# Optimization experiments

Hardware: AMD Instinct MI355X
Metric: run time of the kernel (lower is better)

Reference implementation:

```python
import jax, jax.numpy as jnp
import numpy as np

N_NODES = 50000


def _relgraphconv(x, W, Wloop, b, src, dst, etypes, n_nodes):
    # DGL RelGraphConv (regularizer=None, self_loop=True, norm=None):
    # out[i] = sum over incoming edges (j->i, rel r) of W_r @ x[j]  +  W_loop @ x[i]  +  b
    # low-mem form: transform all nodes per relation, then gather per edge.
    h_rel = jnp.einsum('ni,rio->rno', x, W)          # [R, N, out]
    msg = h_rel[etypes, src]                          # [E, out]
    agg = jax.ops.segment_sum(msg, dst, num_segments=n_nodes)  # [N, out]
    return agg + x @ Wloop + b


def setup_inputs() -> dict:
    key = jax.random.key(0)
    ks = jax.random.split(key, 12)
    N, E, n_state = N_NODES, 800000, 128
    inp = {
        'x': jax.random.normal(ks[0], (N, n_state), dtype=jnp.float32),
        'src': jax.random.randint(ks[1], (E,), 0, N, dtype=jnp.int32),
        'dst': jax.random.randint(ks[2], (E,), 0, N, dtype=jnp.int32),
        'etypes': jax.random.randint(ks[3], (E,), 0, 2, dtype=jnp.int32),
        'cell_size': jax.random.randint(ks[4], (N,), 0, 8, dtype=jnp.int32),
        'max_size': jax.random.randint(ks[5], (N,), 0, 8, dtype=jnp.int32),
        'W1': jax.random.normal(ks[6], (2, n_state, 64), dtype=jnp.float32) * 0.05,
        'loop1': jax.random.normal(ks[7], (n_state, 64), dtype=jnp.float32) * 0.05,
        'b1': jnp.zeros((64,), dtype=jnp.float32),
        'W2': jax.random.normal(ks[8], (2, 64, 64), dtype=jnp.float32) * 0.05,
        'loop2': jax.random.normal(ks[9], (64, 64), dtype=jnp.float32) * 0.05,
        'b2': jnp.zeros((64,), dtype=jnp.float32),
        'W3': jax.random.normal(ks[10], (2, 64, 2), dtype=jnp.float32) * 0.05,
        'loop3': jax.random.normal(ks[11], (64, 2), dtype=jnp.float32) * 0.05,
        'b3': jnp.zeros((2,), dtype=jnp.float32),
    }
    return inp


def reference(x, src, dst, etypes, cell_size, max_size,
              W1, loop1, b1, W2, loop2, b2, W3, loop3, b3):
    N = x.shape[0]
    h = jax.nn.relu(_relgraphconv(x, W1, loop1, b1, src, dst, etypes, N))
    h = jax.nn.relu(_relgraphconv(h, W2, loop2, b2, src, dst, etypes, N))
    h = _relgraphconv(h, W3, loop3, b3, src, dst, etypes, N)   # [N, 2]
    # action mask: col 0 = cannot upsize, col 1 = cannot downsize
    upper = cell_size >= (max_size - 1)
    lower = cell_size == 0
    mask = jnp.stack([upper, lower], axis=1)                   # [N, 2] bool
    return jnp.where(mask, h.min() - 1.0, h)
```

## Files before the change

kernel.cpp:

```cpp
#include <hip/hip_runtime.h>


#define STRIDE 64
#define BINCAP 2560

typedef unsigned short ushortT;
typedef __attribute__((ext_vector_type(8))) short short8;
typedef __attribute__((ext_vector_type(4))) float f32x4;

__device__ inline ushortT f2bf(float f) {
    union { float f; unsigned u; } v; v.f = f;
    unsigned r = v.u + 0x7FFFu + ((v.u >> 16) & 1u);
    return (ushortT)(r >> 16);
}
__device__ inline float bf2f(ushortT h) {
    union { unsigned u; float f; } v; v.u = ((unsigned)h) << 16;
    return v.f;
}

__device__ inline void atomicMinF(float* addr, float v) {
    if (v >= 0.f) atomicMin((int*)addr, __float_as_int(v));
    else          atomicMax((unsigned int*)addr, __float_as_uint(v));
}

__global__ __launch_bounds__(256) void pack_init_kernel(
    const float* __restrict__ W1, const float* __restrict__ loop1,
    const float* __restrict__ W2, const float* __restrict__ loop2,
    ushortT* __restrict__ BP1, ushortT* __restrict__ BP2,
    int* __restrict__ bincnt, float* __restrict__ minval, int NBINS) {
    int g = (int)blockIdx.x * 256 + (int)threadIdx.x;
    if (g < NBINS) bincnt[g] = 0;
    if (g == 0) *(int*)minval = 0x7f7f7f7f;
    if (g < 3072) {
        int l = g & 63, ks = (g >> 6) & 3, ct = g >> 8;
        int c = ct * 16 + (l & 15);
        int mat = c >> 6, cc = c & 63;
        int kbase = ks * 32 + (l >> 4) * 8;
        ushortT* dstp = BP1 + (size_t)g * 8;
#pragma unroll
        for (int j = 0; j < 8; ++j) {
            int k = kbase + j;
            float v = (mat < 2) ? W1[((size_t)mat * 128 + k) * 64 + cc]
                                : loop1[(size_t)k * 64 + cc];
            dstp[j] = f2bf(v);
        }
    } else {
        int s = g - 3072;
        int l = s & 63, ks = (s >> 6) & 1, ct = s >> 7;
        int c = ct * 16 + (l & 15);
        int mat = c >> 6, cc = c & 63;
        int kbase = ks * 32 + (l >> 4) * 8;
        ushortT* dstp = BP2 + (size_t)s * 8;
#pragma unroll
        for (int j = 0; j < 8; ++j) {
            int k = kbase + j;
            float v = (mat < 2) ? W2[((size_t)mat * 64 + k) * 64 + cc]
                                : loop2[(size_t)k * 64 + cc];
            dstp[j] = f2bf(v);
        }
    }
}

__global__ __launch_bounds__(256) void k1_kernel(
    const float* __restrict__ x, const ushortT* __restrict__ BP1,
    const float* __restrict__ b1,
    ushortT* __restrict__ hrelb, ushortT* __restrict__ H1b,
    const int* __restrict__ src, const int* __restrict__ dst,
    const int* __restrict__ et, int* __restrict__ bincnt, int2* __restrict__ binbuf,
    int N, int E, int NBINS, int NBA) {
    __shared__ int hist[512];
    __shared__ int gbase[512];
    __shared__ ushortT rnk[4096];

    const int t = (int)threadIdx.x;

    if ((int)blockIdx.x < NBA) {
        for (int i = t; i < NBINS; i += 256) hist[i] = 0;
        __syncthreads();
        const int base = (int)blockIdx.x * 4096;
#pragma unroll
        for (int i = 0; i < 16; ++i) {
            int e = base + t + i * 256;
            if (e < E) {
                int bb = dst[e] >> 7;
                rnk[t + i * 256] = (ushortT)atomicAdd(&hist[bb], 1);
            }
        }
        __syncthreads();
        for (int i = t; i < NBINS; i += 256) {
            int h = hist[i];
            gbase[i] = h ? atomicAdd(&bincnt[i], h) : 0;
        }
        __syncthreads();
#pragma unroll
        for (int i = 0; i < 16; ++i) {
            int e = base + t + i * 256;
            if (e < E) {
                int dd = dst[e];
                int bb = dd >> 7;
                int v = et[e] * N + src[e];
                int pos = gbase[bb] + (int)rnk[t + i * 256];
                if (pos < BINCAP)
                    binbuf[(size_t)bb * BINCAP + pos] = make_int2(dd, v);
            }
        }
        return;
    }
    const int w = t >> 6, lane = t & 63;
    const int rowbase = (((int)blockIdx.x - NBA) * 4 + w) * 16;
    const int m = lane & 15, quad = lane >> 4;
    const int nclamp = min(rowbase + m, N - 1);

    short8 a[4];
    const float* xp = x + (size_t)nclamp * 128 + quad * 8;
#pragma unroll
    for (int ks = 0; ks < 4; ++ks) {
        float4 g0 = *(const float4*)(xp + ks * 32);
        float4 g1 = *(const float4*)(xp + ks * 32 + 4);
        a[ks][0] = (short)f2bf(g0.x); a[ks][1] = (short)f2bf(g0.y);
        a[ks][2] = (short)f2bf(g0.z); a[ks][3] = (short)f2bf(g0.w);
        a[ks][4] = (short)f2bf(g1.x); a[ks][5] = (short)f2bf(g1.y);
        a[ks][6] = (short)f2bf(g1.z); a[ks][7] = (short)f2bf(g1.w);
    }

    f32x4 acc[12];
#pragma unroll
    for (int ct = 0; ct < 12; ++ct) acc[ct] = (f32x4){0.f, 0.f, 0.f, 0.f};

#pragma unroll
    for (int ks = 0; ks < 4; ++ks) {
#pragma unroll
        for (int ct = 0; ct < 12; ++ct) {
            short8 b = *(const short8*)&BP1[((size_t)(ct * 4 + ks) * 64 + lane) * 8];
            acc[ct] = __builtin_amdgcn_mfma_f32_16x16x32_bf16(a[ks], b, acc[ct], 0, 0, 0);
        }
    }

    const int node0 = rowbase + quad * 4;
#pragma unroll
    for (int ct = 0; ct < 12; ++ct) {
        int c = ct * 16 + m;
        int mat = c >> 6, cc = c & 63;
        float bias = (mat == 2) ? b1[cc] : 0.f;
#pragma unroll
        for (int j = 0; j < 4; ++j) {
            int n = node0 + j;
            if (n < N) {
                float v = acc[ct][j] + bias;
                if (mat < 2) hrelb[((size_t)mat * N + n) * 64 + cc] = f2bf(v);
                else         H1b[(size_t)n * 64 + cc] = f2bf(v);
            }
        }
    }
}

__global__ __launch_bounds__(256) void phaseB_kernel(
    const int* __restrict__ bincnt, const int2* __restrict__ binbuf,
    int* __restrict__ cnt, int* __restrict__ eidx, int N) {
    __shared__ int lcnt[128];
    const int b = (int)blockIdx.x;
    const int t = (int)threadIdx.x;
    if (t < 128) lcnt[t] = 0;
    __syncthreads();
    const int cb = min(bincnt[b], BINCAP);
    const int2* buf = binbuf + (size_t)b * BINCAP;
    for (int i = t; i < cb; i += 256) {
        int2 rec = buf[i];
        int r = atomicAdd(&lcnt[rec.x & 127], 1);
        if (r < STRIDE) eidx[(size_t)rec.x * STRIDE + r] = rec.y;
    }
    __syncthreads();
    int node = b * 128 + t;
    if (t < 128 && node < N) cnt[node] = min(lcnt[t], STRIDE);
}

__global__ void agg1_kernel(const ushortT* __restrict__ hrelb, const int* __restrict__ eidx,
                            const int* __restrict__ cnt, ushortT* __restrict__ H1b, int N) {
    int node = (int)blockIdx.x * 4 + ((int)threadIdx.x >> 6);
    if (node >= N) return;
    int lane = (int)threadIdx.x & 63;
    int deg = cnt[node];
    int my = (lane < deg) ? eidx[(size_t)node * STRIDE + lane] : 0;
    float acc = bf2f(H1b[(size_t)node * 64 + lane]);
    int j = 0;
    for (; j + 7 < deg; j += 8) {
        int id[8];
        float v[8];
#pragma unroll
        for (int q = 0; q < 8; ++q) id[q] = __shfl(my, j + q, 64);
#pragma unroll
        for (int q = 0; q < 8; ++q) v[q] = bf2f(hrelb[(size_t)id[q] * 64 + lane]);
        acc += ((v[0] + v[1]) + (v[2] + v[3])) + ((v[4] + v[5]) + (v[6] + v[7]));
    }
    for (; j < deg; ++j)
        acc += bf2f(hrelb[(size_t)__shfl(my, j, 64) * 64 + lane]);
    H1b[(size_t)node * 64 + lane] = f2bf(fmaxf(acc, 0.f));
}

__global__ __launch_bounds__(256) void gemm2_mfma(
    const ushortT* __restrict__ H1b, const ushortT* __restrict__ BP2,
    const float* __restrict__ b2,
    ushortT* __restrict__ hrel2b, ushortT* __restrict__ H2b, int N) {
    const int w = (int)threadIdx.x >> 6, lane = (int)threadIdx.x & 63;
    const int rowbase = ((int)blockIdx.x * 4 + w) * 16;
    const int m = lane & 15, quad = lane >> 4;
    const int nclamp = min(rowbase + m, N - 1);

    short8 a[2];
    const ushortT* hp = H1b + (size_t)nclamp * 64 + quad * 8;
    a[0] = *(const short8*)(hp);
    a[1] = *(const short8*)(hp + 32);

    f32x4 acc[12];
#pragma unroll
    for (int ct = 0; ct < 12; ++ct) acc[ct] = (f32x4){0.f, 0.f, 0.f, 0.f};

#pragma unroll
    for (int ks = 0; ks < 2; ++ks) {
#pragma unroll
        for (int ct = 0; ct < 12; ++ct) {
            short8 b = *(const short8*)&BP2[((size_t)(ct * 2 + ks) * 64 + lane) * 8];
            acc[ct] = __builtin_amdgcn_mfma_f32_16x16x32_bf16(a[ks], b, acc[ct], 0, 0, 0);
        }
    }

    const int node0 = rowbase + quad * 4;
#pragma unroll
    for (int ct = 0; ct < 12; ++ct) {
        int c = ct * 16 + m;
        int mat = c >> 6, cc = c & 63;
        float bias = (mat == 2) ? b2[cc] : 0.f;
#pragma unroll
        for (int j = 0; j < 4; ++j) {
            int n = node0 + j;
            if (n < N) {
                float v = acc[ct][j] + bias;
                if (mat < 2) hrel2b[((size_t)mat * N + n) * 64 + cc] = f2bf(v);
                else         H2b[(size_t)n * 64 + cc] = f2bf(v);
            }
        }
    }
}

__global__ void k3_kernel(const ushortT* __restrict__ hrel2b, const ushortT* __restrict__ H2b,
                          const int* __restrict__ eidx, const int* __restrict__ cnt,
                          const float* __restrict__ W3, const float* __restrict__ loop3,
                          const float* __restrict__ b3,
                          float* __restrict__ hrel3, float* __restrict__ H3, int N) {
    int node = (int)blockIdx.x * 4 + ((int)threadIdx.x >> 6);
    if (node >= N) return;
    int lane = (int)threadIdx.x & 63;
    int deg = cnt[node];
    int my = (lane < deg) ? eidx[(size_t)node * STRIDE + lane] : 0;
    float acc = bf2f(H2b[(size_t)node * 64 + lane]);
    int j = 0;
    for (; j + 7 < deg; j += 8) {
        int id[8];
        float v[8];
#pragma unroll
        for (int q = 0; q < 8; ++q) id[q] = __shfl(my, j + q, 64);
#pragma unroll
        for (int q = 0; q < 8; ++q) v[q] = bf2f(hrel2b[(size_t)id[q] * 64 + lane]);
        acc += ((v[0] + v[1]) + (v[2] + v[3])) + ((v[4] + v[5]) + (v[6] + v[7]));
    }
    for (; j < deg; ++j)
        acc += bf2f(hrel2b[(size_t)__shfl(my, j, 64) * 64 + lane]);
    float xk = fmaxf(acc, 0.f);
    float p[6];
    p[0] = xk * W3[lane * 2 + 0];
    p[1] = xk * W3[lane * 2 + 1];
    p[2] = xk * W3[(64 + lane) * 2 + 0];
    p[3] = xk * W3[(64 + lane) * 2 + 1];
    p[4] = xk * loop3[lane * 2 + 0];
    p[5] = xk * loop3[lane * 2 + 1];
#pragma unroll
    for (int mm = 32; mm >= 1; mm >>= 1) {
#pragma unroll
        for (int q = 0; q < 6; ++q) p[q] += __shfl_xor(p[q], mm, 64);
    }
    if (lane == 0) {
        hrel3[(size_t)node * 2 + 0] = p[0];
        hrel3[(size_t)node * 2 + 1] = p[1];
        hrel3[((size_t)N + node) * 2 + 0] = p[2];
        hrel3[((size_t)N + node) * 2 + 1] = p[3];
        H3[(size_t)node * 2 + 0] = p[4] + b3[0];
        H3[(size_t)node * 2 + 1] = p[5] + b3[1];
    }
}

__global__ void agg3min_kernel(const float* __restrict__ hrel3, const int* __restrict__ eidx,
                               const int* __restrict__ cnt, float* __restrict__ H3,
                               float* __restrict__ minval, int N) {
    int n = (int)blockIdx.x * 256 + (int)threadIdx.x;
    float v = 3.4e38f;
    if (n < N) {
        float a0 = H3[n * 2 + 0], a1 = H3[n * 2 + 1];
        int deg = cnt[n];
        const int* row = &eidx[(size_t)n * STRIDE];
        int j = 0;
        for (; j + 3 < deg; j += 4) {
            int i0 = row[j], i1 = row[j + 1], i2 = row[j + 2], i3 = row[j + 3];
            float2 q0 = *(const float2*)&hrel3[(size_t)i0 * 2];
            float2 q1 = *(const float2*)&hrel3[(size_t)i1 * 2];
            float2 q2 = *(const float2*)&hrel3[(size_t)i2 * 2];
            float2 q3 = *(const float2*)&hrel3[(size_t)i3 * 2];
            a0 += (q0.x + q1.x) + (q2.x + q3.x);
            a1 += (q0.y + q1.y) + (q2.y + q3.y);
        }
        for (; j < deg; ++j) {
            float2 q = *(const float2*)&hrel3[(size_t)row[j] * 2];
            a0 += q.x; a1 += q.y;
        }
        H3[n * 2 + 0] = a0;
        H3[n * 2 + 1] = a1;
        v = fminf(a0, a1);
    }
#pragma unroll
    for (int mm = 32; mm >= 1; mm >>= 1) v = fminf(v, __shfl_xor(v, mm, 64));
    __shared__ float s[4];
    if ((threadIdx.x & 63) == 0) s[threadIdx.x >> 6] = v;
    __syncthreads();
    if (threadIdx.x == 0)
        atomicMinF(minval, fminf(fminf(s[0], s[1]), fminf(s[2], s[3])));
}

__global__ void mask_kernel(const float* __restrict__ H3, const float* __restrict__ minval,
                            const int* __restrict__ cs, const int* __restrict__ ms,
                            float* __restrict__ out, int N) {
    int n = (int)blockIdx.x * 256 + (int)threadIdx.x;
    if (n >= N) return;
    float m = minval[0] - 1.0f;
    bool up = cs[n] >= ms[n] - 1;
    bool lo = cs[n] == 0;
    out[n * 2 + 0] = up ? m : H3[n * 2 + 0];
    out[n * 2 + 1] = lo ? m : H3[n * 2 + 1];
}

extern "C" void kernel_launch(void* const* d_in, const int* in_sizes, int n_in,
                              void* d_out, int out_size, void* d_ws, size_t ws_size,
                              hipStream_t stream) {
    const float* x     = (const float*)d_in[0];
    const int* src     = (const int*)d_in[1];
    const int* dst     = (const int*)d_in[2];
    const int* etypes  = (const int*)d_in[3];
    const int* cellsz  = (const int*)d_in[4];
    const int* maxsz   = (const int*)d_in[5];
    const float* W1    = (const float*)d_in[6];
    const float* loop1 = (const float*)d_in[7];
    const float* b1    = (const float*)d_in[8];
    const float* W2    = (const float*)d_in[9];
    const float* loop2 = (const float*)d_in[10];
    const float* b2    = (const float*)d_in[11];
    const float* W3    = (const float*)d_in[12];
    const float* loop3 = (const float*)d_in[13];
    const float* b3    = (const float*)d_in[14];
    float* out = (float*)d_out;

    const int N = in_sizes[0] / 128;
    const int E = in_sizes[1];

    char* p = (char*)d_ws;
    auto alloc = [&](size_t bytes) -> void* {
        void* r = (void*)p;
        p += ((bytes + 255) / 256) * 256;
        return r;
    };
    ushortT* hrelb  = (ushortT*)alloc((size_t)2 * N * 64 * 2);
    ushortT* H1b    = (ushortT*)alloc((size_t)N * 64 * 2);
    ushortT* hrel2b = (ushortT*)alloc((size_t)2 * N * 64 * 2);
    ushortT* H2b    = (ushortT*)alloc((size_t)N * 64 * 2);
    float* hrel3    = (float*)alloc((size_t)2 * N * 2 * 4);
    float* H3       = (float*)alloc((size_t)N * 2 * 4);
    int* cnt        = (int*)alloc((size_t)N * 4);
    int* eidx       = (int*)alloc((size_t)N * STRIDE * 4);
    ushortT* BP1    = (ushortT*)alloc((size_t)3072 * 8 * 2);
    ushortT* BP2    = (ushortT*)alloc((size_t)1536 * 8 * 2);
    float* minval   = (float*)alloc(4);

    const int NBINS = (N + 127) >> 7;
    int* bincnt     = (int*)alloc((size_t)NBINS * 4);
    int2* binbuf    = (int2*)alloc((size_t)NBINS * BINCAP * 8);
    (void)ws_size; (void)n_in; (void)out_size;

    const int NB_N   = (N + 255) / 256;
    const int NTILES = (N + 63) / 64;
    const int NB_W   = (N + 3) / 4;
    const int NBA    = (E + 4095) / 4096;

    pack_init_kernel<<<18, 256, 0, stream>>>(
        W1, loop1, W2, loop2, BP1, BP2, bincnt, minval, NBINS);

    k1_kernel<<<NBA + NTILES, 256, 0, stream>>>(
        x, BP1, b1, hrelb, H1b,
        src, dst, etypes, bincnt, binbuf, N, E, NBINS, NBA);

    phaseB_kernel<<<NBINS, 256, 0, stream>>>(bincnt, binbuf, cnt, eidx, N);

    agg1_kernel<<<NB_W, 256, 0, stream>>>(hrelb, eidx, cnt, H1b, N);

    gemm2_mfma<<<NTILES, 256, 0, stream>>>(H1b, BP2, b2, hrel2b, H2b, N);

    k3_kernel<<<NB_W, 256, 0, stream>>>(hrel2b, H2b, eidx, cnt, W3, loop3, b3,
                                        hrel3, H3, N);

    agg3min_kernel<<<NB_N, 256, 0, stream>>>(hrel3, eidx, cnt, H3, minval, N);
    mask_kernel<<<NB_N, 256, 0, stream>>>(H3, minval, cellsz, maxsz, out, N);
}
```

Baseline: 220.4 us.

## Fuse edge binning, layer-1 aggregation and layer-2 GEMM; fuse final min with mask

```diff
diff --git a/kernel.cpp b/kernel.cpp
--- a/kernel.cpp
+++ b/kernel.cpp
@@ -27,10 +27,11 @@
     const float* __restrict__ W1, const float* __restrict__ loop1,
     const float* __restrict__ W2, const float* __restrict__ loop2,
     ushortT* __restrict__ BP1, ushortT* __restrict__ BP2,
-    int* __restrict__ bincnt, float* __restrict__ minval, int NBINS) {
+    int* __restrict__ bincnt, float* __restrict__ minval,
+    int* __restrict__ done, int NBINS) {
     int g = (int)blockIdx.x * 256 + (int)threadIdx.x;
     if (g < NBINS) bincnt[g] = 0;
-    if (g == 0) *(int*)minval = 0x7f7f7f7f;
+    if (g == 0) { *(int*)minval = 0x7f7f7f7f; *done = 0; }
     if (g < 3072) {
         int l = g & 63, ks = (g >> 6) & 3, ct = g >> 8;
         int c = ct * 16 + (l & 15);
@@ -154,79 +155,95 @@
     }
 }
 
-__global__ __launch_bounds__(256) void phaseB_kernel(
+__global__ __launch_bounds__(512, 4) void ag2_kernel(
+    const ushortT* __restrict__ hrelb, const ushortT* __restrict__ H1b,
+    const ushortT* __restrict__ BP2, const float* __restrict__ b2,
     const int* __restrict__ bincnt, const int2* __restrict__ binbuf,
-    int* __restrict__ cnt, int* __restrict__ eidx, int N) {
-    __shared__ int lcnt[128];
-    const int b = (int)blockIdx.x;
+    int* __restrict__ eidx, int* __restrict__ cnt,
+    ushortT* __restrict__ hrel2b, ushortT* __restrict__ H2b, int N) {
+    __shared__ int lcnt[64];
+    __shared__ int lidx[64][STRIDE];
+    __shared__ __align__(16) ushortT Hs[64][72];
+
     const int t = (int)threadIdx.x;
-    if (t < 128) lcnt[t] = 0;
-    __syncthreads();
-    const int cb = min(bincnt[b], BINCAP);
-    const int2* buf = binbuf + (size_t)b * BINCAP;
-    for (int i = t; i < cb; i += 256) {
+    const int B = (int)blockIdx.x;
+    const int nodeBase = B * 64;
+    const int bin = B >> 1;
+
+    if (t < 64) lcnt[t] = 0;
+    __syncthreads();
+
+    const int cb = min(bincnt[bin], BINCAP);
+    const int2* buf = binbuf + (size_t)bin * BINCAP;
+    for (int i = t; i < cb; i += 512) {
         int2 rec = buf[i];
-        int r = atomicAdd(&lcnt[rec.x & 127], 1);
-        if (r < STRIDE) eidx[(size_t)rec.x * STRIDE + r] = rec.y;
-    }
-    __syncthreads();
-    int node = b * 128 + t;
-    if (t < 128 && node < N) cnt[node] = min(lcnt[t], STRIDE);
-}
-
-__global__ void agg1_kernel(const ushortT* __restrict__ hrelb, const int* __restrict__ eidx,
-                            const int* __restrict__ cnt, ushortT* __restrict__ H1b, int N) {
-    int node = (int)blockIdx.x * 4 + ((int)threadIdx.x >> 6);
-    if (node >= N) return;
-    int lane = (int)threadIdx.x & 63;
-    int deg = cnt[node];
-    int my = (lane < deg) ? eidx[(size_t)node * STRIDE + lane] : 0;
-    float acc = bf2f(H1b[(size_t)node * 64 + lane]);
-    int j = 0;
-    for (; j + 7 < deg; j += 8) {
-        int id[8];
-        float v[8];
-#pragma unroll
-        for (int q = 0; q < 8; ++q) id[q] = __shfl(my, j + q, 64);
-#pragma unroll
-        for (int q = 0; q < 8; ++q) v[q] = bf2f(hrelb[(size_t)id[q] * 64 + lane]);
-        acc += ((v[0] + v[1]) + (v[2] + v[3])) + ((v[4] + v[5]) + (v[6] + v[7]));
-    }
-    for (; j < deg; ++j)
-        acc += bf2f(hrelb[(size_t)__shfl(my, j, 64) * 64 + lane]);
-    H1b[(size_t)node * 64 + lane] = f2bf(fmaxf(acc, 0.f));
-}
-
-__global__ __launch_bounds__(256) void gemm2_mfma(
-    const ushortT* __restrict__ H1b, const ushortT* __restrict__ BP2,
-    const float* __restrict__ b2,
-    ushortT* __restrict__ hrel2b, ushortT* __restrict__ H2b, int N) {
-    const int w = (int)threadIdx.x >> 6, lane = (int)threadIdx.x & 63;
-    const int rowbase = ((int)blockIdx.x * 4 + w) * 16;
+        int local = rec.x - nodeBase;
+        if ((unsigned)local < 64u) {
+            int r = atomicAdd(&lcnt[local], 1);
+            if (r < STRIDE) {
+                lidx[local][r] = rec.y;
+                eidx[(size_t)rec.x * STRIDE + r] = rec.y;
+            }
+        }
+    }
+    __syncthreads();
+    if (t < 64) {
+        int c = min(lcnt[t], STRIDE);
+        lcnt[t] = c;
+        int node = nodeBase + t;
+        if (node < N) cnt[node] = c;
+    }
+    __syncthreads();
+
+    const int w = t >> 6, lane = t & 63;
+
+    for (int i = 0; i < 8; ++i) {
+        int local = w * 8 + i;
+        int node = nodeBase + local;
+        if (node >= N) { Hs[local][lane] = 0; continue; }
+        int deg = lcnt[local];
+        float acc = bf2f(H1b[(size_t)node * 64 + lane]);
+        int j = 0;
+        for (; j + 7 < deg; j += 8) {
+            float v[8];
+#pragma unroll
+            for (int q = 0; q < 8; ++q) {
+                int id = lidx[local][j + q];
+                v[q] = bf2f(hrelb[(size_t)id * 64 + lane]);
+            }
+            acc += ((v[0] + v[1]) + (v[2] + v[3])) + ((v[4] + v[5]) + (v[6] + v[7]));
+        }
+        for (; j < deg; ++j)
+            acc += bf2f(hrelb[(size_t)lidx[local][j] * 64 + lane]);
+        Hs[local][lane] = f2bf(fmaxf(acc, 0.f));
+    }
+    __syncthreads();
+
+    const int rt = w & 3, h = w >> 2;
     const int m = lane & 15, quad = lane >> 4;
-    const int nclamp = min(rowbase + m, N - 1);
-
     short8 a[2];
-    const ushortT* hp = H1b + (size_t)nclamp * 64 + quad * 8;
-    a[0] = *(const short8*)(hp);
-    a[1] = *(const short8*)(hp + 32);
-
-    f32x4 acc[12];
-#pragma unroll
-    for (int ct = 0; ct < 12; ++ct) acc[ct] = (f32x4){0.f, 0.f, 0.f, 0.f};
+#pragma unroll
+    for (int ks = 0; ks < 2; ++ks)
+        a[ks] = *(const short8*)&Hs[rt * 16 + m][quad * 8 + ks * 32];
+
+    f32x4 acc[6];
+#pragma unroll
+    for (int c6 = 0; c6 < 6; ++c6) acc[c6] = (f32x4){0.f, 0.f, 0.f, 0.f};
 
 #pragma unroll
     for (int ks = 0; ks < 2; ++ks) {
 #pragma unroll
-        for (int ct = 0; ct < 12; ++ct) {
+        for (int c6 = 0; c6 < 6; ++c6) {
+            int ct = h * 6 + c6;
             short8 b = *(const short8*)&BP2[((size_t)(ct * 2 + ks) * 64 + lane) * 8];
-            acc[ct] = __builtin_amdgcn_mfma_f32_16x16x32_bf16(a[ks], b, acc[ct], 0, 0, 0);
-        }
-    }
-
-    const int node0 = rowbase + quad * 4;
-#pragma unroll
-    for (int ct = 0; ct < 12; ++ct) {
+            acc[c6] = __builtin_amdgcn_mfma_f32_16x16x32_bf16(a[ks], b, acc[c6], 0, 0, 0);
+        }
+    }
+
+    const int node0 = nodeBase + rt * 16 + quad * 4;
+#pragma unroll
+    for (int c6 = 0; c6 < 6; ++c6) {
+        int ct = h * 6 + c6;
         int c = ct * 16 + m;
         int mat = c >> 6, cc = c & 63;
         float bias = (mat == 2) ? b2[cc] : 0.f;
@@ -234,7 +251,7 @@
         for (int j = 0; j < 4; ++j) {
             int n = node0 + j;
             if (n < N) {
-                float v = acc[ct][j] + bias;
+                float v = acc[c6][j] + bias;
                 if (mat < 2) hrel2b[((size_t)mat * N + n) * 64 + cc] = f2bf(v);
                 else         H2b[(size_t)n * 64 + cc] = f2bf(v);
             }
@@ -288,13 +305,18 @@
     }
 }
 
-__global__ void agg3min_kernel(const float* __restrict__ hrel3, const int* __restrict__ eidx,
-                               const int* __restrict__ cnt, float* __restrict__ H3,
-                               float* __restrict__ minval, int N) {
-    int n = (int)blockIdx.x * 256 + (int)threadIdx.x;
+__global__ __launch_bounds__(256) void a3m_mask_kernel(
+    const float* __restrict__ hrel3, const int* __restrict__ eidx,
+    const int* __restrict__ cnt, const float* __restrict__ H3,
+    const int* __restrict__ cs, const int* __restrict__ ms,
+    float* __restrict__ minval, int* __restrict__ done,
+    float* __restrict__ out, int N) {
+    const int t = (int)threadIdx.x;
+    const int n = (int)blockIdx.x * 256 + t;
+    float a0 = 0.f, a1 = 0.f;
     float v = 3.4e38f;
     if (n < N) {
-        float a0 = H3[n * 2 + 0], a1 = H3[n * 2 + 1];
+        a0 = H3[n * 2 + 0]; a1 = H3[n * 2 + 1];
         int deg = cnt[n];
         const int* row = &eidx[(size_t)n * STRIDE];
         int j = 0;
@@ -311,29 +333,30 @@
             float2 q = *(const float2*)&hrel3[(size_t)row[j] * 2];
             a0 += q.x; a1 += q.y;
         }
-        H3[n * 2 + 0] = a0;
-        H3[n * 2 + 1] = a1;
         v = fminf(a0, a1);
     }
 #pragma unroll
     for (int mm = 32; mm >= 1; mm >>= 1) v = fminf(v, __shfl_xor(v, mm, 64));
     __shared__ float s[4];
-    if ((threadIdx.x & 63) == 0) s[threadIdx.x >> 6] = v;
-    __syncthreads();
-    if (threadIdx.x == 0)
+    __shared__ float gm;
+    if ((t & 63) == 0) s[t >> 6] = v;
+    __syncthreads();
+    if (t == 0) {
         atomicMinF(minval, fminf(fminf(s[0], s[1]), fminf(s[2], s[3])));
-}
-
-__global__ void mask_kernel(const float* __restrict__ H3, const float* __restrict__ minval,
-                            const int* __restrict__ cs, const int* __restrict__ ms,
-                            float* __restrict__ out, int N) {
-    int n = (int)blockIdx.x * 256 + (int)threadIdx.x;
-    if (n >= N) return;
-    float m = minval[0] - 1.0f;
-    bool up = cs[n] >= ms[n] - 1;
-    bool lo = cs[n] == 0;
-    out[n * 2 + 0] = up ? m : H3[n * 2 + 0];
-    out[n * 2 + 1] = lo ? m : H3[n * 2 + 1];
+        __threadfence();
+        atomicAdd(done, 1);
+        while (atomicAdd(done, 0) < (int)gridDim.x)
+            __builtin_amdgcn_s_sleep(2);
+        gm = atomicAdd(minval, 0.0f);
+    }
+    __syncthreads();
+    if (n < N) {
+        float mn = gm - 1.0f;
+        bool up = cs[n] >= ms[n] - 1;
+        bool lo = cs[n] == 0;
+        out[n * 2 + 0] = up ? mn : a0;
+        out[n * 2 + 1] = lo ? mn : a1;
+    }
 }
 
 extern "C" void kernel_launch(void* const* d_in, const int* in_sizes, int n_in,
@@ -376,6 +399,7 @@
     ushortT* BP1    = (ushortT*)alloc((size_t)3072 * 8 * 2);
     ushortT* BP2    = (ushortT*)alloc((size_t)1536 * 8 * 2);
     float* minval   = (float*)alloc(4);
+    int* done       = (int*)alloc(4);
 
     const int NBINS = (N + 127) >> 7;
     int* bincnt     = (int*)alloc((size_t)NBINS * 4);
@@ -386,23 +410,21 @@
     const int NTILES = (N + 63) / 64;
     const int NB_W   = (N + 3) / 4;
     const int NBA    = (E + 4095) / 4096;
+    const int NB_AG  = (N + 63) / 64;
 
     pack_init_kernel<<<18, 256, 0, stream>>>(
-        W1, loop1, W2, loop2, BP1, BP2, bincnt, minval, NBINS);
+        W1, loop1, W2, loop2, BP1, BP2, bincnt, minval, done, NBINS);
 
     k1_kernel<<<NBA + NTILES, 256, 0, stream>>>(
         x, BP1, b1, hrelb, H1b,
         src, dst, etypes, bincnt, binbuf, N, E, NBINS, NBA);
 
-    phaseB_kernel<<<NBINS, 256, 0, stream>>>(bincnt, binbuf, cnt, eidx, N);
-
-    agg1_kernel<<<NB_W, 256, 0, stream>>>(hrelb, eidx, cnt, H1b, N);
-
-    gemm2_mfma<<<NTILES, 256, 0, stream>>>(H1b, BP2, b2, hrel2b, H2b, N);
+    ag2_kernel<<<NB_AG, 512, 0, stream>>>(
+        hrelb, H1b, BP2, b2, bincnt, binbuf, eidx, cnt, hrel2b, H2b, N);
 
     k3_kernel<<<NB_W, 256, 0, stream>>>(hrel2b, H2b, eidx, cnt, W3, loop3, b3,
                                         hrel3, H3, N);
 
-    agg3min_kernel<<<NB_N, 256, 0, stream>>>(hrel3, eidx, cnt, H3, minval, N);
-    mask_kernel<<<NB_N, 256, 0, stream>>>(H3, minval, cellsz, maxsz, out, N);
-}
+    a3m_mask_kernel<<<NB_N, 256, 0, stream>>>(hrel3, eidx, cnt, H3,
+                                              cellsz, maxsz, minval, done, out, N);
+}
```

Result: no change. 219.1 us, median of 2 (-0.6%).

## Slice relation messages into 8-channel chunks and fuse min/mask with grid barrier

Applied to the files above, without the earlier changes.

```diff
diff --git a/kernel.cpp b/kernel.cpp
--- a/kernel.cpp
+++ b/kernel.cpp
@@ -27,10 +27,11 @@
     const float* __restrict__ W1, const float* __restrict__ loop1,
     const float* __restrict__ W2, const float* __restrict__ loop2,
     ushortT* __restrict__ BP1, ushortT* __restrict__ BP2,
-    int* __restrict__ bincnt, float* __restrict__ minval, int NBINS) {
+    int* __restrict__ bincnt, float* __restrict__ minval,
+    int* __restrict__ done, int NBINS) {
     int g = (int)blockIdx.x * 256 + (int)threadIdx.x;
     if (g < NBINS) bincnt[g] = 0;
-    if (g == 0) *(int*)minval = 0x7f7f7f7f;
+    if (g == 0) { *(int*)minval = 0x7f7f7f7f; *done = 0; }
     if (g < 3072) {
         int l = g & 63, ks = (g >> 6) & 3, ct = g >> 8;
         int c = ct * 16 + (l & 15);
@@ -64,7 +65,7 @@
 __global__ __launch_bounds__(256) void k1_kernel(
     const float* __restrict__ x, const ushortT* __restrict__ BP1,
     const float* __restrict__ b1,
-    ushortT* __restrict__ hrelb, ushortT* __restrict__ H1b,
+    ushortT* __restrict__ hrelbS, ushortT* __restrict__ H1b,
     const int* __restrict__ src, const int* __restrict__ dst,
     const int* __restrict__ et, int* __restrict__ bincnt, int2* __restrict__ binbuf,
     int N, int E, int NBINS, int NBA) {
@@ -73,6 +74,7 @@
     __shared__ ushortT rnk[4096];
 
     const int t = (int)threadIdx.x;
+    const size_t N2 = (size_t)2 * N;
 
     if ((int)blockIdx.x < NBA) {
         for (int i = t; i < NBINS; i += 256) hist[i] = 0;
@@ -147,8 +149,10 @@
             int n = node0 + j;
             if (n < N) {
                 float v = acc[ct][j] + bias;
-                if (mat < 2) hrelb[((size_t)mat * N + n) * 64 + cc] = f2bf(v);
-                else         H1b[(size_t)n * 64 + cc] = f2bf(v);
+                if (mat < 2)
+                    hrelbS[((size_t)(cc >> 3) * N2 + (size_t)mat * N + n) * 8 + (cc & 7)] = f2bf(v);
+                else
+                    H1b[(size_t)n * 64 + cc] = f2bf(v);
             }
         }
     }
@@ -174,37 +178,66 @@
     if (t < 128 && node < N) cnt[node] = min(lcnt[t], STRIDE);
 }
 
-__global__ void agg1_kernel(const ushortT* __restrict__ hrelb, const int* __restrict__ eidx,
-                            const int* __restrict__ cnt, ushortT* __restrict__ H1b, int N) {
-    int node = (int)blockIdx.x * 4 + ((int)threadIdx.x >> 6);
+__global__ __launch_bounds__(256) void agg_slice_kernel(
+    const ushortT* __restrict__ msgS, const int* __restrict__ eidx,
+    const int* __restrict__ cnt, ushortT* __restrict__ H, int N) {
+    const int b = (int)blockIdx.x;
+    const int s = b & 7;
+    const int t = (int)threadIdx.x;
+    const int w = t >> 6, lane = t & 63;
+    const int g = lane >> 3, ch8 = lane & 7;
+    const int node = (b >> 3) * 32 + w * 8 + g;
     if (node >= N) return;
-    int lane = (int)threadIdx.x & 63;
-    int deg = cnt[node];
-    int my = (lane < deg) ? eidx[(size_t)node * STRIDE + lane] : 0;
-    float acc = bf2f(H1b[(size_t)node * 64 + lane]);
-    int j = 0;
-    for (; j + 7 < deg; j += 8) {
-        int id[8];
-        float v[8];
-#pragma unroll
-        for (int q = 0; q < 8; ++q) id[q] = __shfl(my, j + q, 64);
-#pragma unroll
-        for (int q = 0; q < 8; ++q) v[q] = bf2f(hrelb[(size_t)id[q] * 64 + lane]);
-        acc += ((v[0] + v[1]) + (v[2] + v[3])) + ((v[4] + v[5]) + (v[6] + v[7]));
-    }
-    for (; j < deg; ++j)
-        acc += bf2f(hrelb[(size_t)__shfl(my, j, 64) * 64 + lane]);
-    H1b[(size_t)node * 64 + lane] = f2bf(fmaxf(acc, 0.f));
+
+    const int deg = cnt[node];
+    const ushortT* base = msgS + (size_t)s * 2 * N * 8;
+    const int* row = eidx + (size_t)node * STRIDE;
+
+    float acc[8] = {0.f, 0.f, 0.f, 0.f, 0.f, 0.f, 0.f, 0.f};
+    for (int e = ch8; e < deg; e += 8) {
+        int id = row[e];
+        uint4 rv = *(const uint4*)(base + (size_t)id * 8);
+        acc[0] += bf2f((ushortT)(rv.x & 0xffff));
+        acc[1] += bf2f((ushortT)(rv.x >> 16));
+        acc[2] += bf2f((ushortT)(rv.y & 0xffff));
+        acc[3] += bf2f((ushortT)(rv.y >> 16));
+        acc[4] += bf2f((ushortT)(rv.z & 0xffff));
+        acc[5] += bf2f((ushortT)(rv.z >> 16));
+        acc[6] += bf2f((ushortT)(rv.w & 0xffff));
+        acc[7] += bf2f((ushortT)(rv.w >> 16));
+    }
+    float a4[4];
+#pragma unroll
+    for (int q = 0; q < 4; ++q) {
+        float sendv = (ch8 & 1) ? acc[2 * q] : acc[2 * q + 1];
+        float keepv = (ch8 & 1) ? acc[2 * q + 1] : acc[2 * q];
+        a4[q] = keepv + __shfl_xor(sendv, 1, 64);
+    }
+    float a2[2];
+#pragma unroll
+    for (int q = 0; q < 2; ++q) {
+        float sendv = (ch8 & 2) ? a4[2 * q] : a4[2 * q + 1];
+        float keepv = (ch8 & 2) ? a4[2 * q + 1] : a4[2 * q];
+        a2[q] = keepv + __shfl_xor(sendv, 2, 64);
+    }
+    float sendv = (ch8 & 4) ? a2[0] : a2[1];
+    float keepv = (ch8 & 4) ? a2[1] : a2[0];
+    float tot = keepv + __shfl_xor(sendv, 4, 64);
+
+    size_t hoff = (size_t)node * 64 + s * 8 + ch8;
+    float r = fmaxf(bf2f(H[hoff]) + tot, 0.f);
+    H[hoff] = f2bf(r);
 }
 
 __global__ __launch_bounds__(256) void gemm2_mfma(
     const ushortT* __restrict__ H1b, const ushortT* __restrict__ BP2,
     const float* __restrict__ b2,
-    ushortT* __restrict__ hrel2b, ushortT* __restrict__ H2b, int N) {
+    ushortT* __restrict__ hrel2bS, ushortT* __restrict__ H2b, int N) {
     const int w = (int)threadIdx.x >> 6, lane = (int)threadIdx.x & 63;
     const int rowbase = ((int)blockIdx.x * 4 + w) * 16;
     const int m = lane & 15, quad = lane >> 4;
     const int nclamp = min(rowbase + m, N - 1);
+    const size_t N2 = (size_t)2 * N;
 
     short8 a[2];
     const ushortT* hp = H1b + (size_t)nclamp * 64 + quad * 8;
@@ -235,37 +268,23 @@
             int n = node0 + j;
             if (n < N) {
                 float v = acc[ct][j] + bias;
-                if (mat < 2) hrel2b[((size_t)mat * N + n) * 64 + cc] = f2bf(v);
-                else         H2b[(size_t)n * 64 + cc] = f2bf(v);
+                if (mat < 2)
+                    hrel2bS[((size_t)(cc >> 3) * N2 + (size_t)mat * N + n) * 8 + (cc & 7)] = f2bf(v);
+                else
+                    H2b[(size_t)n * 64 + cc] = f2bf(v);
             }
         }
     }
 }
 
-__global__ void k3_kernel(const ushortT* __restrict__ hrel2b, const ushortT* __restrict__ H2b,
-                          const int* __restrict__ eidx, const int* __restrict__ cnt,
-                          const float* __restrict__ W3, const float* __restrict__ loop3,
-                          const float* __restrict__ b3,
-                          float* __restrict__ hrel3, float* __restrict__ H3, int N) {
+__global__ void k3p_kernel(const ushortT* __restrict__ H2b,
+                           const float* __restrict__ W3, const float* __restrict__ loop3,
+                           const float* __restrict__ b3,
+                           float* __restrict__ hrel3, float* __restrict__ H3, int N) {
     int node = (int)blockIdx.x * 4 + ((int)threadIdx.x >> 6);
     if (node >= N) return;
     int lane = (int)threadIdx.x & 63;
-    int deg = cnt[node];
-    int my = (lane < deg) ? eidx[(size_t)node * STRIDE + lane] : 0;
-    float acc = bf2f(H2b[(size_t)node * 64 + lane]);
-    int j = 0;
-    for (; j + 7 < deg; j += 8) {
-        int id[8];
-        float v[8];
-#pragma unroll
-        for (int q = 0; q < 8; ++q) id[q] = __shfl(my, j + q, 64);
-#pragma unroll
-        for (int q = 0; q < 8; ++q) v[q] = bf2f(hrel2b[(size_t)id[q] * 64 + lane]);
-        acc += ((v[0] + v[1]) + (v[2] + v[3])) + ((v[4] + v[5]) + (v[6] + v[7]));
-    }
-    for (; j < deg; ++j)
-        acc += bf2f(hrel2b[(size_t)__shfl(my, j, 64) * 64 + lane]);
-    float xk = fmaxf(acc, 0.f);
+    float xk = bf2f(H2b[(size_t)node * 64 + lane]);
     float p[6];
     p[0] = xk * W3[lane * 2 + 0];
     p[1] = xk * W3[lane * 2 + 1];
@@ -288,13 +307,18 @@
     }
 }
 
-__global__ void agg3min_kernel(const float* __restrict__ hrel3, const int* __restrict__ eidx,
-                               const int* __restrict__ cnt, float* __restrict__ H3,
-                               float* __restrict__ minval, int N) {
-    int n = (int)blockIdx.x * 256 + (int)threadIdx.x;
+__global__ __launch_bounds__(256) void a3m_mask_kernel(
+    const float* __restrict__ hrel3, const int* __restrict__ eidx,
+    const int* __restrict__ cnt, const float* __restrict__ H3,
+    const int* __restrict__ cs, const int* __restrict__ ms,
+    float* __restrict__ minval, int* __restrict__ done,
+    float* __restrict__ out, int N) {
+    const int t = (int)threadIdx.x;
+    const int n = (int)blockIdx.x * 256 + t;
+    float a0 = 0.f, a1 = 0.f;
     float v = 3.4e38f;
     if (n < N) {
-        float a0 = H3[n * 2 + 0], a1 = H3[n * 2 + 1];
+        a0 = H3[n * 2 + 0]; a1 = H3[n * 2 + 1];
         int deg = cnt[n];
         const int* row = &eidx[(size_t)n * STRIDE];
         int j = 0;
@@ -311,29 +335,30 @@
             float2 q = *(const float2*)&hrel3[(size_t)row[j] * 2];
             a0 += q.x; a1 += q.y;
         }
-        H3[n * 2 + 0] = a0;
-        H3[n * 2 + 1] = a1;
         v = fminf(a0, a1);
     }
 #pragma unroll
     for (int mm = 32; mm >= 1; mm >>= 1) v = fminf(v, __shfl_xor(v, mm, 64));
     __shared__ float s[4];
-    if ((threadIdx.x & 63) == 0) s[threadIdx.x >> 6] = v;
+    __shared__ float gm;
+    if ((t & 63) == 0) s[t >> 6] = v;
     __syncthreads();
-    if (threadIdx.x == 0)
+    if (t == 0) {
         atomicMinF(minval, fminf(fminf(s[0], s[1]), fminf(s[2], s[3])));
-}
-
-__global__ void mask_kernel(const float* __restrict__ H3, const float* __restrict__ minval,
-                            const int* __restrict__ cs, const int* __restrict__ ms,
-                            float* __restrict__ out, int N) {
-    int n = (int)blockIdx.x * 256 + (int)threadIdx.x;
-    if (n >= N) return;
-    float m = minval[0] - 1.0f;
-    bool up = cs[n] >= ms[n] - 1;
-    bool lo = cs[n] == 0;
-    out[n * 2 + 0] = up ? m : H3[n * 2 + 0];
-    out[n * 2 + 1] = lo ? m : H3[n * 2 + 1];
+        __threadfence();
+        atomicAdd(done, 1);
+        while (atomicAdd(done, 0) < (int)gridDim.x)
+            __builtin_amdgcn_s_sleep(2);
+        gm = atomicAdd(minval, 0.0f);
+    }
+    __syncthreads();
+    if (n < N) {
+        float mn = gm - 1.0f;
+        bool up = cs[n] >= ms[n] - 1;
+        bool lo = cs[n] == 0;
+        out[n * 2 + 0] = up ? mn : a0;
+        out[n * 2 + 1] = lo ? mn : a1;
+    }
 }
 
 extern "C" void kernel_launch(void* const* d_in, const int* in_sizes, int n_in,
@@ -365,17 +390,18 @@
         p += ((bytes + 255) / 256) * 256;
         return r;
     };
-    ushortT* hrelb  = (ushortT*)alloc((size_t)2 * N * 64 * 2);
-    ushortT* H1b    = (ushortT*)alloc((size_t)N * 64 * 2);
-    ushortT* hrel2b = (ushortT*)alloc((size_t)2 * N * 64 * 2);
-    ushortT* H2b    = (ushortT*)alloc((size_t)N * 64 * 2);
-    float* hrel3    = (float*)alloc((size_t)2 * N * 2 * 4);
-    float* H3       = (float*)alloc((size_t)N * 2 * 4);
-    int* cnt        = (int*)alloc((size_t)N * 4);
-    int* eidx       = (int*)alloc((size_t)N * STRIDE * 4);
-    ushortT* BP1    = (ushortT*)alloc((size_t)3072 * 8 * 2);
-    ushortT* BP2    = (ushortT*)alloc((size_t)1536 * 8 * 2);
-    float* minval   = (float*)alloc(4);
+    ushortT* hrelbS  = (ushortT*)alloc((size_t)2 * N * 64 * 2);
+    ushortT* H1b     = (ushortT*)alloc((size_t)N * 64 * 2);
+    ushortT* hrel2bS = (ushortT*)alloc((size_t)2 * N * 64 * 2);
+    ushortT* H2b     = (ushortT*)alloc((size_t)N * 64 * 2);
+    float* hrel3     = (float*)alloc((size_t)2 * N * 2 * 4);
+    float* H3        = (float*)alloc((size_t)N * 2 * 4);
+    int* cnt         = (int*)alloc((size_t)N * 4);
+    int* eidx        = (int*)alloc((size_t)N * STRIDE * 4);
+    ushortT* BP1     = (ushortT*)alloc((size_t)3072 * 8 * 2);
+    ushortT* BP2     = (ushortT*)alloc((size_t)1536 * 8 * 2);
+    float* minval    = (float*)alloc(4);
+    int* done        = (int*)alloc(4);
 
     const int NBINS = (N + 127) >> 7;
     int* bincnt     = (int*)alloc((size_t)NBINS * 4);
@@ -386,23 +412,25 @@
     const int NTILES = (N + 63) / 64;
     const int NB_W   = (N + 3) / 4;
     const int NBA    = (E + 4095) / 4096;
+    const int NB_AGG = ((N + 31) / 32) * 8;
 
     pack_init_kernel<<<18, 256, 0, stream>>>(
-        W1, loop1, W2, loop2, BP1, BP2, bincnt, minval, NBINS);
+        W1, loop1, W2, loop2, BP1, BP2, bincnt, minval, done, NBINS);
 
     k1_kernel<<<NBA + NTILES, 256, 0, stream>>>(
-        x, BP1, b1, hrelb, H1b,
+        x, BP1, b1, hrelbS, H1b,
         src, dst, etypes, bincnt, binbuf, N, E, NBINS, NBA);
 
     phaseB_kernel<<<NBINS, 256, 0, stream>>>(bincnt, binbuf, cnt, eidx, N);
 
-    agg1_kernel<<<NB_W, 256, 0, stream>>>(hrelb, eidx, cnt, H1b, N);
-
-    gemm2_mfma<<<NTILES, 256, 0, stream>>>(H1b, BP2, b2, hrel2b, H2b, N);
-
-    k3_kernel<<<NB_W, 256, 0, stream>>>(hrel2b, H2b, eidx, cnt, W3, loop3, b3,
-                                        hrel3, H3, N);
-
-    agg3min_kernel<<<NB_N, 256, 0, stream>>>(hrel3, eidx, cnt, H3, minval, N);
-    mask_kernel<<<NB_N, 256, 0, stream>>>(H3, minval, cellsz, maxsz, out, N);
-}
+    agg_slice_kernel<<<NB_AGG, 256, 0, stream>>>(hrelbS, eidx, cnt, H1b, N);
+
+    gemm2_mfma<<<NTILES, 256, 0, stream>>>(H1b, BP2, b2, hrel2bS, H2b, N);
+
+    agg_slice_kernel<<<NB_AGG, 256, 0, stream>>>(hrel2bS, eidx, cnt, H2b, N);
+
+    k3p_kernel<<<NB_W, 256, 0, stream>>>(H2b, W3, loop3, b3, hrel3, H3, N);
+
+    a3m_mask_kernel<<<NB_N, 256, 0, stream>>>(hrel3, eidx, cnt, H3,
+                                              cellsz, maxsz, minval, done, out, N);
+}
```

After: 276.6 us. 1.25x slower.
